# Optimization experiments

Measured on AMD Instinct MI355X. Metric: run time of the kernel, lower is better.

## Reference

```python
import jax, jax.numpy as jnp
import numpy as np
import math

ATTN_C = 32
HEADS = 8
IN_C = 256
PAIR_C = 128
B, M, N = 1, 128, 256


def _layernorm(x, w, b, eps=1e-5):
    mu = jnp.mean(x, axis=-1, keepdims=True)
    xc = x - mu
    var = jnp.mean(xc * xc, axis=-1, keepdims=True)
    return xc * jax.lax.rsqrt(var + eps) * w + b


def setup_inputs() -> dict:
    key = jax.random.key(0)
    ks = jax.random.split(key, 10)
    s1 = 1.0 / math.sqrt(IN_C)
    s2 = 1.0 / math.sqrt(PAIR_C)
    s3 = 1.0 / math.sqrt(ATTN_C * HEADS)
    return {
        "x1d": jax.random.normal(ks[0], (B, M, N, IN_C), jnp.float32),
        "x2d": jax.random.normal(ks[1], (B, N, N, PAIR_C), jnp.float32),
        "norm_w": jnp.ones((IN_C,), jnp.float32),
        "norm_b": jnp.zeros((IN_C,), jnp.float32),
        "qkv_w": jax.random.normal(ks[2], (3 * ATTN_C * HEADS, IN_C), jnp.float32) * s1,
        "x2d_w": jax.random.normal(ks[3], (HEADS, PAIR_C), jnp.float32) * s2,
        "gate_w": jax.random.normal(ks[4], (ATTN_C * HEADS, IN_C), jnp.float32) * s1,
        "gate_b": jnp.zeros((ATTN_C * HEADS,), jnp.float32),
        "final_w": jax.random.normal(ks[5], (IN_C, ATTN_C * HEADS), jnp.float32) * s3,
        "final_b": jnp.zeros((IN_C,), jnp.float32),
    }


def reference(x1d, x2d, norm_w, norm_b, qkv_w, x2d_w, gate_w, gate_b, final_w, final_b):
    c, h = ATTN_C, HEADS
    x = _layernorm(x1d, norm_w, norm_b)                      # [B,M,N,IN_C]
    qkv = (x @ qkv_w.T).reshape(*x.shape[:-1], c, 3 * h)     # [B,M,N,c,3h]
    q, k, v = qkv[..., :h], qkv[..., h:2 * h], qkv[..., 2 * h:]
    aff = jnp.einsum('bmich,bmjch->bmijh', q, k)             # [B,M,N,N,H]
    gate = jax.nn.sigmoid(x @ gate_w.T + gate_b).reshape(*x.shape[:-1], c, h)
    factor = 1.0 / math.sqrt(c)
    bias = (x2d @ x2d_w.T) * factor                          # [B,N,N,H]
    weights = jax.nn.softmax(aff + bias[:, None], axis=-2)   # softmax over j
    out = jnp.einsum('bmrch,bmirh->bmich', v, weights) * gate
    out = out.reshape(*x.shape[:-1], c * h) @ final_w.T + final_b
    return out
```

## Files before the change

### kernel.cpp

```cpp
#include <hip/hip_runtime.h>
#include <math.h>

typedef short bf16x8 __attribute__((ext_vector_type(8)));
typedef float f32x4  __attribute__((ext_vector_type(4)));

#define NPOS 32768
#define LOG2E 1.4426950408889634f

#define OFF_AHI   100663296u
#define OFF_ATTN  134217728u
#define OFF_BIAST 150994944u
#define OFF_WHI   153354240u
#define OFF_W2P   154402816u
#define OFF_GBP   154533888u

__device__ __forceinline__ short f2bf(float x) {
    unsigned int u = __float_as_uint(x);
    unsigned int r = (u + 0x7FFFu + ((u >> 16) & 1u)) >> 16;
    return (short)r;
}
__device__ __forceinline__ float bf2f(short s) {
    return __uint_as_float(((unsigned int)(unsigned short)s) << 16);
}
__device__ __forceinline__ void async_copy16(const void* g, void* l) {
    __builtin_amdgcn_global_load_lds(
        (const __attribute__((address_space(1))) unsigned int*)g,
        (__attribute__((address_space(3))) unsigned int*)l, 16, 0, 0);
}

#define PREP_LN   8192
#define PREP_CW   9473
__global__ __launch_bounds__(256) void k_prep(
    const float* __restrict__ x, const float* __restrict__ nw, const float* __restrict__ nb,
    const float* __restrict__ qkvw, const float* __restrict__ gatew,
    const float* __restrict__ gateb, const float* __restrict__ finalw,
    const float* __restrict__ x2d, const float* __restrict__ x2dw,
    short* __restrict__ Ahi, short* __restrict__ Whi, short* __restrict__ W2p,
    float* __restrict__ gbp, float* __restrict__ biasT) {
    __shared__ float xs[64][132];
    __shared__ float ws[8][132];
    const int bid = blockIdx.x;
    const int t = threadIdx.x;

    if (bid < PREP_LN) {
        int wid = (bid * 256 + t) >> 6;
        int lane = t & 63;
        const float4 v = ((const float4*)(x + (size_t)wid * 256))[lane];
        float s  = v.x + v.y + v.z + v.w;
        float ss = v.x*v.x + v.y*v.y + v.z*v.z + v.w*v.w;
        #pragma unroll
        for (int o = 32; o; o >>= 1) {
            s  += __shfl_xor(s,  o, 64);
            ss += __shfl_xor(ss, o, 64);
        }
        float mu  = s * (1.0f / 256);
        float var = ss * (1.0f / 256) - mu * mu;
        float rs  = rsqrtf(var + 1e-5f);
        const float4 wv = ((const float4*)nw)[lane];
        const float4 bv = ((const float4*)nb)[lane];
        float y[4] = {(v.x - mu) * rs * wv.x + bv.x, (v.y - mu) * rs * wv.y + bv.y,
                      (v.z - mu) * rs * wv.z + bv.z, (v.w - mu) * rs * wv.w + bv.w};
        short h4[4];
        #pragma unroll
        for (int i = 0; i < 4; ++i) h4[i] = f2bf(y[i]);
        *(short4*)(Ahi + (size_t)wid * 256 + lane * 4) = *(short4*)h4;
    } else if (bid < PREP_CW) {
        int r = bid - PREP_LN;
        if (r < 1024) {
            int which = r >> 8, h = (r >> 5) & 7, c = r & 31;
            const float* src = (which < 3) ? qkvw + (size_t)(c * 24 + which * 8 + h) * 256
                                           : gatew + (size_t)(c * 8 + h) * 256;
            Whi[(size_t)r * 256 + t] = f2bf(src[t]);
        } else if (r < 1280) {
            int o = r - 1024;
            int h = t >> 5, c = t & 31;
            W2p[(size_t)o * 256 + t] = f2bf(finalw[(size_t)o * 256 + c * 8 + h]);
        } else {
            int h = t >> 5, c = t & 31;
            gbp[t] = gateb[c * 8 + h];
        }
    } else {
        const int wid0 = (bid - PREP_CW) * 64;
        #pragma unroll
        for (int r = 0; r < 8; ++r) {
            int g = r * 256 + t;
            int row = g >> 5, c4 = g & 31;
            float4 v = *(const float4*)(x2d + (size_t)(wid0 + row) * 128 + c4 * 4);
            *(float4*)&xs[row][c4 * 4] = v;
        }
        {
            int h = t >> 5, c4 = t & 31;
            *(float4*)&ws[h][c4 * 4] = *(const float4*)(x2dw + h * 128 + c4 * 4);
        }
        __syncthreads();
        const float f = 0.17677669529663687f * LOG2E;
        const int i = wid0 >> 8;
        #pragma unroll
        for (int kk = 0; kk < 2; ++kk) {
            int o = t + kk * 256;
            int row = o >> 3, h = o & 7;
            float acc = 0.f;
            #pragma unroll
            for (int c4 = 0; c4 < 32; ++c4) {
                float4 xv = *(const float4*)&xs[row][c4 * 4];
                float4 wv = *(const float4*)&ws[h][c4 * 4];
                acc += xv.x * wv.x + xv.y * wv.y + xv.z * wv.z + xv.w * wv.w;
            }
            int j = (wid0 & 255) + row;
            biasT[(((h * 256 + j)) << 8) + i] = acc * f;
        }
    }
}

__global__ __launch_bounds__(512, 4) void k_fused(
    const short* __restrict__ Ahi, const short* __restrict__ Whi,
    const float* __restrict__ gbp, const float* __restrict__ biasT,
    short* __restrict__ attnB) {
    __shared__ __align__(16) short smem[38144];
    short* As  = smem;
    short* Ws  = smem + 16384;
    short* Khi = smem;
    short* VT  = smem + 8192;
    short* Qs  = smem + 16640;
    short* Gs  = smem + 24832;
    short* Pl  = smem + 33024;

    const int mh = blockIdx.x;
    const int h = mh >> 7, m = mh & 127;
    const int t = threadIdx.x;
    const int wave = t >> 6, lane = t & 63, ln15 = lane & 15, quad = lane >> 4;
    const int i0 = wave * 32;

    f32x4 acc[2][8];
    #pragma unroll
    for (int a = 0; a < 2; ++a)
        #pragma unroll
        for (int b = 0; b < 8; ++b) acc[a][b] = (f32x4){0.f, 0.f, 0.f, 0.f};

    for (int k0 = 0; k0 < 256; k0 += 64) {
        #pragma unroll
        for (int r = 0; r < 4; ++r) {
            int g = r * 512 + t;
            int row = g >> 3, cs = g & 7;
            int colg = cs ^ (row & 7);
            async_copy16(Ahi + (size_t)(m * 256 + row) * 256 + k0 + colg * 8, &As[g * 8]);
        }
        #pragma unroll
        for (int r = 0; r < 2; ++r) {
            int g = r * 512 + t;
            int row = g >> 3, cs = g & 7;
            int colg = cs ^ (row & 7);
            int nrow = (row >> 5) * 256 + h * 32 + (row & 31);
            async_copy16(Whi + (size_t)nrow * 256 + k0 + colg * 8, &Ws[g * 8]);
        }
        __syncthreads();
        #pragma unroll
        for (int kc = 0; kc < 2; ++kc) {
            bf16x8 af[2], bfr[8];
            #pragma unroll
            for (int it = 0; it < 2; ++it) {
                int rowa = i0 + it * 16 + ln15;
                int c8a = (kc * 4 + quad) ^ (rowa & 7);
                af[it] = *(const bf16x8*)&As[rowa * 64 + c8a * 8];
            }
            #pragma unroll
            for (int nt = 0; nt < 8; ++nt) {
                int rowb = nt * 16 + ln15;
                int c8b = (kc * 4 + quad) ^ (rowb & 7);
                bfr[nt] = *(const bf16x8*)&Ws[rowb * 64 + c8b * 8];
            }
            #pragma unroll
            for (int it = 0; it < 2; ++it)
                #pragma unroll
                for (int nt = 0; nt < 8; ++nt)
                    acc[it][nt] = __builtin_amdgcn_mfma_f32_16x16x32_bf16(
                        bfr[nt], af[it], acc[it][nt], 0, 0, 0);
        }
        __syncthreads();
    }

    #pragma unroll
    for (int it = 0; it < 2; ++it) {
        int j = i0 + it * 16 + ln15;
        int sw = j & 3;
        #pragma unroll
        for (int nt = 0; nt < 8; ++nt) {
            int which = nt >> 1;
            int cloc0 = (nt & 1) * 16 + quad * 4;
            float v0 = acc[it][nt][0], v1 = acc[it][nt][1];
            float v2 = acc[it][nt][2], v3 = acc[it][nt][3];
            if (which == 3) {
                const float4 gb = *(const float4*)&gbp[h * 32 + cloc0];
                v0 = 1.0f / (1.0f + __expf(-(v0 + gb.x)));
                v1 = 1.0f / (1.0f + __expf(-(v1 + gb.y)));
                v2 = 1.0f / (1.0f + __expf(-(v2 + gb.z)));
                v3 = 1.0f / (1.0f + __expf(-(v3 + gb.w)));
            }
            short s0 = f2bf(v0), s1 = f2bf(v1), s2 = f2bf(v2), s3 = f2bf(v3);
            if (which == 2) {
                VT[(cloc0 + 0) * 264 + j] = s0;
                VT[(cloc0 + 1) * 264 + j] = s1;
                VT[(cloc0 + 2) * 264 + j] = s2;
                VT[(cloc0 + 3) * 264 + j] = s3;
            } else {
                unsigned w0 = (unsigned)(unsigned short)s0 | ((unsigned)(unsigned short)s1 << 16);
                unsigned w1 = (unsigned)(unsigned short)s2 | ((unsigned)(unsigned short)s3 << 16);
                int cg = cloc0 >> 3, off = cloc0 & 7;
                short* dst = (which == 0) ? &Qs[j * 32 + (cg ^ sw) * 8 + off]
                           : (which == 1) ? &Khi[j * 32 + (cg ^ sw) * 8 + off]
                                          : &Gs[j * 32 + cloc0];
                *(uint2*)dst = make_uint2(w0, w1);
            }
        }
    }
    __syncthreads();

    bf16x8 qhi[2];
    #pragma unroll
    for (int it = 0; it < 2; ++it) {
        int i = i0 + it * 16 + ln15;
        qhi[it] = *(const bf16x8*)&Qs[i * 32 + ((quad ^ (i & 3))) * 8];
    }
    float lacc[2] = {0.f, 0.f};
    f32x4 Oacc[2][2];
    #pragma unroll
    for (int a = 0; a < 2; ++a) {
        Oacc[a][0] = (f32x4){0.f, 0.f, 0.f, 0.f};
        Oacc[a][1] = (f32x4){0.f, 0.f, 0.f, 0.f};
    }
    const float* bp = biasT + (size_t)h * 65536;

    for (int j0 = 0; j0 < 256; j0 += 32) {
        bf16x8 kfh[2], vf[2];
        #pragma unroll
        for (int jt = 0; jt < 2; ++jt) {
            int j = j0 + jt * 16 + ln15;
            int cs = quad ^ (j & 3);
            kfh[jt] = *(const bf16x8*)&Khi[j * 32 + cs * 8];
        }
        #pragma unroll
        for (int ct = 0; ct < 2; ++ct) {
            int c = ct * 16 + ln15;
            vf[ct] = *(const bf16x8*)&VT[c * 264 + j0 + quad * 8];
        }
        #pragma unroll
        for (int it = 0; it < 2; ++it) {
            int i = i0 + it * 16 + ln15;
            float b0[4], b1[4];
            #pragma unroll
            for (int r = 0; r < 4; ++r) {
                b0[r] = bp[(j0 + quad * 4 + r) * 256 + i];
                b1[r] = bp[(j0 + 16 + quad * 4 + r) * 256 + i];
            }
            f32x4 s0 = (f32x4){0.f, 0.f, 0.f, 0.f};
            f32x4 s1 = (f32x4){0.f, 0.f, 0.f, 0.f};
            s0 = __builtin_amdgcn_mfma_f32_16x16x32_bf16(kfh[0], qhi[it], s0, 0, 0, 0);
            s1 = __builtin_amdgcn_mfma_f32_16x16x32_bf16(kfh[1], qhi[it], s1, 0, 0, 0);
            float p[8], ps = 0.f;
            #pragma unroll
            for (int r = 0; r < 4; ++r) {
                p[r] = __builtin_amdgcn_exp2f(fmaf(s0[r], LOG2E, b0[r]));
                ps += p[r];
            }
            #pragma unroll
            for (int r = 0; r < 4; ++r) {
                p[4 + r] = __builtin_amdgcn_exp2f(fmaf(s1[r], LOG2E, b1[r]));
                ps += p[4 + r];
            }
            lacc[it] += ps;
            unsigned long long pw0 =
                  (unsigned long long)(unsigned short)f2bf(p[0])
                | ((unsigned long long)(unsigned short)f2bf(p[1]) << 16)
                | ((unsigned long long)(unsigned short)f2bf(p[2]) << 32)
                | ((unsigned long long)(unsigned short)f2bf(p[3]) << 48);
            unsigned long long pw1 =
                  (unsigned long long)(unsigned short)f2bf(p[4])
                | ((unsigned long long)(unsigned short)f2bf(p[5]) << 16)
                | ((unsigned long long)(unsigned short)f2bf(p[6]) << 32)
                | ((unsigned long long)(unsigned short)f2bf(p[7]) << 48);
            short* plp = &Pl[(wave * 16 + ln15) * 40];
            *(unsigned long long*)&plp[quad * 4]      = pw0;
            *(unsigned long long*)&plp[16 + quad * 4] = pw1;
            bf16x8 pf = *(const bf16x8*)&plp[quad * 8];
            Oacc[it][0] = __builtin_amdgcn_mfma_f32_16x16x32_bf16(pf, vf[0], Oacc[it][0], 0, 0, 0);
            Oacc[it][1] = __builtin_amdgcn_mfma_f32_16x16x32_bf16(pf, vf[1], Oacc[it][1], 0, 0, 0);
        }
    }
    #pragma unroll
    for (int it = 0; it < 2; ++it) {
        float l = lacc[it];
        l += __shfl_xor(l, 16, 64);
        l += __shfl_xor(l, 32, 64);
        float inv = 1.0f / l;
        float invr[4];
        #pragma unroll
        for (int r = 0; r < 4; ++r) invr[r] = __shfl(inv, quad * 4 + r, 16);
        #pragma unroll
        for (int ct = 0; ct < 2; ++ct) {
            int c = ct * 16 + ln15;
            #pragma unroll
            for (int r = 0; r < 4; ++r) {
                int i = i0 + it * 16 + quad * 4 + r;
                float g = bf2f(Gs[i * 32 + c]);
                float val = Oacc[it][ct][r] * invr[r] * g;
                attnB[(size_t)(m * 256 + i) * 256 + h * 32 + c] = f2bf(val);
            }
        }
    }
}

__global__ __launch_bounds__(256) void k_gemm2m(
    const short* __restrict__ A, const short* __restrict__ W2p,
    const float* __restrict__ fb, float* __restrict__ out) {
    __shared__ short As[128 * 64];
    __shared__ short Bs[128 * 64];
    const int t = threadIdx.x;
    const int wave = t >> 6, lane = t & 63, ln15 = lane & 15, quad = lane >> 4;
    const int posBase = blockIdx.x * 128;
    const int nb = blockIdx.y;
    const int i0w = (wave & 1) * 64, n0w = (wave >> 1) * 64;

    f32x4 acc[4][4];
    #pragma unroll
    for (int a = 0; a < 4; ++a)
        #pragma unroll
        for (int b = 0; b < 4; ++b) acc[a][b] = (f32x4){0.f, 0.f, 0.f, 0.f};

    for (int k0 = 0; k0 < 256; k0 += 64) {
        #pragma unroll
        for (int r = 0; r < 4; ++r) {
            int g = r * 256 + t;
            int row = g >> 3, cs = g & 7;
            int colg = cs ^ (row & 7);
            const short* ga = A + (size_t)(posBase + row) * 256 + k0 + colg * 8;
            async_copy16(ga, &As[(r * 256 + wave * 64) * 8]);
            const short* gb = W2p + (size_t)(nb * 128 + row) * 256 + k0 + colg * 8;
            async_copy16(gb, &Bs[(r * 256 + wave * 64) * 8]);
        }
        __syncthreads();
        #pragma unroll
        for (int kc = 0; kc < 2; ++kc) {
            bf16x8 af[4], bfr[4];
            #pragma unroll
            for (int it = 0; it < 4; ++it) {
                int rowa = i0w + it * 16 + ln15;
                int c8a = (kc * 4 + quad) ^ (rowa & 7);
                af[it] = *(const bf16x8*)&As[rowa * 64 + c8a * 8];
                int rowb = n0w + it * 16 + ln15;
                int c8b = (kc * 4 + quad) ^ (rowb & 7);
                bfr[it] = *(const bf16x8*)&Bs[rowb * 64 + c8b * 8];
            }
            #pragma unroll
            for (int it = 0; it < 4; ++it)
                #pragma unroll
                for (int nt = 0; nt < 4; ++nt)
                    acc[it][nt] = __builtin_amdgcn_mfma_f32_16x16x32_bf16(
                        bfr[nt], af[it], acc[it][nt], 0, 0, 0);
        }
        __syncthreads();
    }
    #pragma unroll
    for (int it = 0; it < 4; ++it) {
        size_t pos = posBase + i0w + it * 16 + ln15;
        #pragma unroll
        for (int nt = 0; nt < 4; ++nt) {
            int ncol0 = nb * 128 + n0w + nt * 16 + quad * 4;
            const float4 fbv = *(const float4*)&fb[ncol0];
            float4 o;
            o.x = acc[it][nt][0] + fbv.x;
            o.y = acc[it][nt][1] + fbv.y;
            o.z = acc[it][nt][2] + fbv.z;
            o.w = acc[it][nt][3] + fbv.w;
            *(float4*)&out[pos * 256 + ncol0] = o;
        }
    }
}

extern "C" void kernel_launch(void* const* d_in, const int* in_sizes, int n_in,
                              void* d_out, int out_size, void* d_ws, size_t ws_size,
                              hipStream_t stream) {
    const float* x1d     = (const float*)d_in[0];
    const float* x2d     = (const float*)d_in[1];
    const float* norm_w  = (const float*)d_in[2];
    const float* norm_b  = (const float*)d_in[3];
    const float* qkv_w   = (const float*)d_in[4];
    const float* x2d_w   = (const float*)d_in[5];
    const float* gate_w  = (const float*)d_in[6];
    const float* gate_b  = (const float*)d_in[7];
    const float* final_w = (const float*)d_in[8];
    const float* final_b = (const float*)d_in[9];
    float* out = (float*)d_out;
    char* w = (char*)d_ws;

    short* Ahi   = (short*)(w + OFF_AHI);
    short* attnB = (short*)(w + OFF_ATTN);
    float* biasT = (float*)(w + OFF_BIAST);
    short* Whi   = (short*)(w + OFF_WHI);
    short* W2p   = (short*)(w + OFF_W2P);
    float* gbp   = (float*)(w + OFF_GBP);

    k_prep<<<10497, 256, 0, stream>>>(x1d, norm_w, norm_b, qkv_w, gate_w, gate_b,
                                      final_w, x2d, x2d_w, Ahi, Whi, W2p, gbp, biasT);
    k_fused<<<1024, 512, 0, stream>>>(Ahi, Whi, gbp, biasT, attnB);
    k_gemm2m<<<dim3(256, 2), 256, 0, stream>>>(attnB, W2p, final_b, out);
}
```

Before: 191.2 us.

## Shrink fused-kernel shared memory by keeping Q and gate per-wave

Drops the block-wide Q and gate shared buffers. Q is staged through each wave's private P scratch row and loaded straight into registers, and the gate values stay packed in registers until the epilogue, where they are staged through the same row. This cuts shared memory from about 76KB to 48KB and raises the launch-bounds occupancy hint from 4 to 6, so more blocks can be resident per CU. The cost is extra registers held across the attention loop for the gate values, plus a tighter register budget from the higher occupancy hint, which may cause spills.

Measured after the change: 374.8 us. +96.0%, slower.

```diff
diff --git a/kernel.cpp b/kernel.cpp
--- a/kernel.cpp
+++ b/kernel.cpp
@@ -112,18 +112,16 @@
     }
 }
 
-__global__ __launch_bounds__(512, 4) void k_fused(
+__global__ __launch_bounds__(512, 6) void k_fused(
     const short* __restrict__ Ahi, const short* __restrict__ Whi,
     const float* __restrict__ gbp, const float* __restrict__ biasT,
     short* __restrict__ attnB) {
-    __shared__ __align__(16) short smem[38144];
+    __shared__ __align__(16) short smem[24576];
     short* As  = smem;
     short* Ws  = smem + 16384;
     short* Khi = smem;
     short* VT  = smem + 8192;
-    short* Qs  = smem + 16640;
-    short* Gs  = smem + 24832;
-    short* Pl  = smem + 33024;
+    short* Pl  = smem + 16640;
 
     const int mh = blockIdx.x;
     const int h = mh >> 7, m = mh & 127;
@@ -179,6 +177,9 @@
         __syncthreads();
     }
 
+    unsigned gpk[2][4];
+    bf16x8 qhi[2];
+    short* plrow = &Pl[(wave * 16 + ln15) * 40];
     #pragma unroll
     for (int it = 0; it < 2; ++it) {
         int j = i0 + it * 16 + ln15;
@@ -205,22 +206,21 @@
             } else {
                 unsigned w0 = (unsigned)(unsigned short)s0 | ((unsigned)(unsigned short)s1 << 16);
                 unsigned w1 = (unsigned)(unsigned short)s2 | ((unsigned)(unsigned short)s3 << 16);
-                int cg = cloc0 >> 3, off = cloc0 & 7;
-                short* dst = (which == 0) ? &Qs[j * 32 + (cg ^ sw) * 8 + off]
-                           : (which == 1) ? &Khi[j * 32 + (cg ^ sw) * 8 + off]
-                                          : &Gs[j * 32 + cloc0];
-                *(uint2*)dst = make_uint2(w0, w1);
-            }
-        }
+                if (which == 0) {
+                    *(uint2*)&plrow[cloc0] = make_uint2(w0, w1);
+                } else if (which == 1) {
+                    int cg = cloc0 >> 3, off = cloc0 & 7;
+                    *(uint2*)&Khi[j * 32 + (cg ^ sw) * 8 + off] = make_uint2(w0, w1);
+                } else {
+                    gpk[it][(nt & 1) * 2]     = w0;
+                    gpk[it][(nt & 1) * 2 + 1] = w1;
+                }
+            }
+        }
+        qhi[it] = *(const bf16x8*)&plrow[quad * 8];
     }
     __syncthreads();
 
-    bf16x8 qhi[2];
-    #pragma unroll
-    for (int it = 0; it < 2; ++it) {
-        int i = i0 + it * 16 + ln15;
-        qhi[it] = *(const bf16x8*)&Qs[i * 32 + ((quad ^ (i & 3))) * 8];
-    }
     float lacc[2] = {0.f, 0.f};
     f32x4 Oacc[2][2];
     #pragma unroll
@@ -278,16 +278,17 @@
                 | ((unsigned long long)(unsigned short)f2bf(p[5]) << 16)
                 | ((unsigned long long)(unsigned short)f2bf(p[6]) << 32)
                 | ((unsigned long long)(unsigned short)f2bf(p[7]) << 48);
-            short* plp = &Pl[(wave * 16 + ln15) * 40];
-            *(unsigned long long*)&plp[quad * 4]      = pw0;
-            *(unsigned long long*)&plp[16 + quad * 4] = pw1;
-            bf16x8 pf = *(const bf16x8*)&plp[quad * 8];
+            *(unsigned long long*)&plrow[quad * 4]      = pw0;
+            *(unsigned long long*)&plrow[16 + quad * 4] = pw1;
+            bf16x8 pf = *(const bf16x8*)&plrow[quad * 8];
             Oacc[it][0] = __builtin_amdgcn_mfma_f32_16x16x32_bf16(pf, vf[0], Oacc[it][0], 0, 0, 0);
             Oacc[it][1] = __builtin_amdgcn_mfma_f32_16x16x32_bf16(pf, vf[1], Oacc[it][1], 0, 0, 0);
         }
     }
     #pragma unroll
     for (int it = 0; it < 2; ++it) {
+        *(uint2*)&plrow[quad * 4]      = make_uint2(gpk[it][0], gpk[it][1]);
+        *(uint2*)&plrow[16 + quad * 4] = make_uint2(gpk[it][2], gpk[it][3]);
         float l = lacc[it];
         l += __shfl_xor(l, 16, 64);
         l += __shfl_xor(l, 32, 64);
@@ -301,7 +302,7 @@
             #pragma unroll
             for (int r = 0; r < 4; ++r) {
                 int i = i0 + it * 16 + quad * 4 + r;
-                float g = bf2f(Gs[i * 32 + c]);
+                float g = bf2f(Pl[(wave * 16 + quad * 4 + r) * 40 + ct * 16 + ln15]);
                 float val = Oacc[it][ct][r] * invr[r] * g;
                 attnB[(size_t)(m * 256 + i) * 256 + h * 32 + c] = f2bf(val);
             }
```
